# Optimization experiments

Measured on AMD Instinct MI355X. Metric: run time of the kernel, lower is better.

The kernel has to match this reference:

```python
import jax, jax.numpy as jnp
import numpy as np

SR = 24000
N_FFT = 2048
WIN = 960
HOP = 240
NUM_BANDS = 150
HID = 128
OUT = 64
LOG_E_MIN = -18.0  # stands in for trained log_energy_min buffer
LOG_E_MAX = 5.0    # stands in for trained log_energy_max buffer
FREQ_INTERVAL = SR / N_FFT


def _stft_power(x):
    # torchaudio Spectrogram(power=2, center=True, pad_mode=reflect)
    pad = N_FFT // 2
    xp = jnp.pad(x, ((0, 0), (pad, pad)), mode='reflect')
    n = jnp.arange(WIN, dtype=jnp.float32)
    win = 0.5 - 0.5 * jnp.cos(2.0 * jnp.pi * n / WIN)  # periodic hann
    lp = (N_FFT - WIN) // 2
    win = jnp.pad(win, (lp, N_FFT - WIN - lp))  # center-pad window to n_fft
    T = 1 + x.shape[1] // HOP
    idx = (jnp.arange(T) * HOP)[:, None] + jnp.arange(N_FFT)[None, :]  # [T, n_fft]
    frames = xp[:, idx] * win  # [B, T, n_fft]
    F = jnp.fft.rfft(frames, axis=-1)  # [B, T, n_fft//2+1]
    return F.real ** 2 + F.imag ** 2


def _lstm_dir(feat_tbd, w_ih, w_hh, b, reverse):
    # feat_tbd: [T, B, D]; PyTorch gate order i, f, g, o
    xs = jnp.flip(feat_tbd, 0) if reverse else feat_tbd
    pre = jnp.einsum('tbd,gd->tbg', xs, w_ih) + b  # input projection hoisted out of scan

    def step(carry, z_in):
        h, c = carry
        z = z_in + h @ w_hh.T
        i, f, g, o = jnp.split(z, 4, axis=-1)
        c = jax.nn.sigmoid(f) * c + jax.nn.sigmoid(i) * jnp.tanh(g)
        h = jax.nn.sigmoid(o) * jnp.tanh(c)
        return (h, c), h

    B = feat_tbd.shape[1]
    h0 = jnp.zeros((B, HID), feat_tbd.dtype)
    _, hs = jax.lax.scan(step, (h0, h0), pre)
    return jnp.flip(hs, 0) if reverse else hs


def setup_inputs() -> dict:
    key = jax.random.key(0)
    ks = jax.random.split(key, 12)
    B, L, T = 16, 240000, 1001
    x = jax.random.normal(ks[0], (B, L), jnp.float32) * 0.1
    f0_raw = jax.random.uniform(ks[1], (B, T), jnp.float32, 50.0, 400.0)
    voiced = jax.random.uniform(ks[2], (B, T)) > 0.1
    f0 = jnp.where(voiced, f0_raw, 0.0)
    D_in = NUM_BANDS * 2 + 1  # 301
    s = 0.08
    return {
        'x': x,
        'f0': f0,
        'w_ih_f': jax.random.normal(ks[3], (4 * HID, D_in), jnp.float32) * s,
        'w_hh_f': jax.random.normal(ks[4], (4 * HID, HID), jnp.float32) * s,
        'b_f': jax.random.normal(ks[5], (4 * HID,), jnp.float32) * s,
        'w_ih_b': jax.random.normal(ks[6], (4 * HID, D_in), jnp.float32) * s,
        'w_hh_b': jax.random.normal(ks[7], (4 * HID, HID), jnp.float32) * s,
        'b_b': jax.random.normal(ks[8], (4 * HID,), jnp.float32) * s,
        'ln_g': jnp.ones((2 * HID,), jnp.float32),
        'ln_b': jnp.zeros((2 * HID,), jnp.float32),
        'out_w': jax.random.normal(ks[9], (OUT, 2 * HID), jnp.float32) * 0.02,
        'out_b': jnp.zeros((OUT,), jnp.float32),
    }


def reference(x, f0, w_ih_f, w_hh_f, b_f, w_ih_b, w_hh_b, b_b, ln_g, ln_b, out_w, out_b):
    spec = _stft_power(x)                     # [B, T, 1025]
    spec = spec.at[..., -1].set(0.0)          # spec[..., -1] = 0
    Tf = min(spec.shape[1], f0.shape[1])
    spec = spec[:, :Tf]
    f0 = f0[:, :Tf]
    f0_nonzero = jnp.where(f0 > 0, f0, SR / NUM_BANDS * 0.5)
    mult = jnp.arange(1.0, NUM_BANDS + 0.5, 0.5, dtype=jnp.float32)  # [299]
    harms = f0_nonzero[..., None] * mult                              # [B, T, 299]
    harms = jnp.concatenate([harms[..., :1] * 0.5, harms], axis=-1)   # [B, T, 300]
    hidx = jnp.clip(jnp.round(harms / FREQ_INTERVAL).astype(jnp.int32), 0, spec.shape[-1] - 1)
    harms_energy = jnp.take_along_axis(spec, hidx, axis=-1)           # irregular gather
    log_energy = jnp.log(harms_energy + 1e-8)
    feature = (log_energy - LOG_E_MIN) / (LOG_E_MAX - LOG_E_MIN)
    feature = jnp.concatenate([feature, jnp.log(f0_nonzero)[..., None]], axis=-1)  # [B, T, 301]
    ft = feature.transpose(1, 0, 2)  # [T, B, 301]
    hf = _lstm_dir(ft, w_ih_f, w_hh_f, b_f, False)
    hb = _lstm_dir(ft, w_ih_b, w_hh_b, b_b, True)
    h = jnp.concatenate([hf, hb], axis=-1).transpose(1, 0, 2)  # [B, T, 256]
    mu = h.mean(-1, keepdims=True)
    var = h.var(-1, keepdims=True)
    hn = (h - mu) / jnp.sqrt(var + 1e-5) * ln_g + ln_b
    return hn @ out_w.T + out_b  # [B, T, 64]
```

## Files before the change

kernel.cpp:

```cpp
#include <hip/hip_runtime.h>

typedef __bf16 bf16x8 __attribute__((ext_vector_type(8)));
typedef float f32x4 __attribute__((ext_vector_type(4)));
typedef int   i32x4 __attribute__((ext_vector_type(4)));

__device__ __forceinline__ void sync_lds() {
    asm volatile("s_waitcnt lgkmcnt(0)" ::: "memory");
    __builtin_amdgcn_s_barrier();
}

__global__ __launch_bounds__(256) void prep_kernel(
    const float* __restrict__ x, const float* __restrict__ w_ih_f, const float* __restrict__ w_ih_b,
    __bf16* __restrict__ BT, __bf16* __restrict__ A, __bf16* __restrict__ WT)
{
    int blk = blockIdx.x;
    if (blk < 7680) {
        int id = blk * 256 + threadIdx.x;
        int n = id / 960;
        int j = id - n * 960;
        int k = n >> 1;
        int p = (k * (544 + j)) & 2047;
        float pr = (float)p * (1.0f / 2048.0f);
        float v = (n & 1) ? __builtin_amdgcn_sinf(pr) : __builtin_amdgcn_cosf(pr);
        BT[id] = (__bf16)v;
    } else if (blk < 37920) {
        int id = (blk - 7680) * 256 + threadIdx.x;
        int frame = id / 480;
        int jp = (id - frame * 480) * 2;
        float v[2] = {0.f, 0.f};
        if (frame < 16016) {
            int b = frame / 1001;
            int t = frame - b * 1001;
            const float* xb = x + (size_t)b * 240000;
            #pragma unroll
            for (int e = 0; e < 2; ++e) {
                int j = jp + e;
                int s = t * 240 + j - 480;
                if (s < 0) s = -s;
                else if (s >= 240000) s = 479998 - s;
                float win = 0.5f - 0.5f * __builtin_amdgcn_cosf((float)j * (1.0f / 960.0f));
                v[e] = xb[s] * win;
            }
        }
        union { unsigned int u; __bf16 h[2]; } pk;
        pk.h[0] = (__bf16)v[0]; pk.h[1] = (__bf16)v[1];
        *reinterpret_cast<unsigned int*>(&A[(size_t)frame * 960 + jp]) = pk.u;
    } else {
        int id = (blk - 37920) * 256 + threadIdx.x;
        int n = id / 320;
        int k = id - n * 320;
        float v = 0.f;
        if (k < 301) v = (n < 512) ? w_ih_f[n * 301 + k] : w_ih_b[(n - 512) * 301 + k];
        WT[id] = (__bf16)v;
    }
}

__global__ __launch_bounds__(256) void gemm_kernel(
    const __bf16* __restrict__ A, const __bf16* __restrict__ BT,
    int Ka, int kIters, int mode,
    __bf16* __restrict__ Cdft, float* __restrict__ pre,
    const float* __restrict__ b_f, const float* __restrict__ b_b)
{
    __shared__ __bf16 As[128 * 64];
    __shared__ __bf16 Bs[128 * 64];
    const int tid = threadIdx.x;
    const int wave = tid >> 6, lane = tid & 63, l15 = lane & 15, quad = lane >> 4;
    const int bn = blockIdx.x, bm = blockIdx.y;
    const int qm = wave >> 1, qn = wave & 1;
    f32x4 acc[4][4] = {};
    const int rl  = lane >> 3;
    const int gch = (lane & 7) ^ rl;
    const __bf16* Ag = A + (size_t)(bm * 128) * Ka;
    const __bf16* Bg = BT + (size_t)(bn * 128) * Ka;

    for (int kb = 0; kb < kIters; ++kb) {
        int k0 = kb * 64;
        #pragma unroll
        for (int p = 0; p < 4; ++p) {
            int c = wave + p * 4;
            int row = c * 8 + rl;
            __builtin_amdgcn_global_load_lds(
                (const __attribute__((address_space(1))) void*)(Ag + (size_t)row * Ka + k0 + gch * 8),
                (__attribute__((address_space(3))) void*)(As + c * 512), 16, 0, 0);
            __builtin_amdgcn_global_load_lds(
                (const __attribute__((address_space(1))) void*)(Bg + (size_t)row * Ka + k0 + gch * 8),
                (__attribute__((address_space(3))) void*)(Bs + c * 512), 16, 0, 0);
        }
        __syncthreads();
        #pragma unroll
        for (int ks = 0; ks < 2; ++ks) {
            bf16x8 af[4], bfr[4];
            #pragma unroll
            for (int i = 0; i < 4; ++i) {
                int row = qm * 64 + i * 16 + l15;
                int ch = (ks * 4 + quad) ^ (l15 & 7);
                af[i] = *reinterpret_cast<const bf16x8*>(&As[row * 64 + ch * 8]);
            }
            #pragma unroll
            for (int j = 0; j < 4; ++j) {
                int row = qn * 64 + j * 16 + l15;
                int ch = (ks * 4 + quad) ^ (l15 & 7);
                bfr[j] = *reinterpret_cast<const bf16x8*>(&Bs[row * 64 + ch * 8]);
            }
            #pragma unroll
            for (int i = 0; i < 4; ++i)
                #pragma unroll
                for (int j = 0; j < 4; ++j)
                    acc[i][j] = __builtin_amdgcn_mfma_f32_16x16x32_bf16(af[i], bfr[j], acc[i][j], 0, 0, 0);
        }
        __syncthreads();
    }

    if (mode == 0) {
        #pragma unroll
        for (int i = 0; i < 4; ++i)
            #pragma unroll
            for (int j = 0; j < 4; ++j) {
                int n = bn * 128 + qn * 64 + j * 16 + l15;
                #pragma unroll
                for (int r = 0; r < 4; ++r) {
                    int m = bm * 128 + qm * 64 + i * 16 + quad * 4 + r;
                    Cdft[(size_t)m * 2048 + n] = (__bf16)acc[i][j][r];
                }
            }
    } else {
        const float L2E = 1.4426950408889634f;
        for (int i = 0; i < 4; ++i)
            for (int j = 0; j < 4; ++j) {
                int n = bn * 128 + qn * 64 + j * 16 + l15;
                float bias = (n < 512) ? b_f[n] : b_b[n - 512];
                int dirg = n >> 9;
                int ngate = n & 511;
                int g = ngate >> 7;
                int jj = ngate & 127;
                float gam = (g == 2) ? (-2.f * L2E) : (-L2E);
                for (int r = 0; r < 4; ++r) {
                    int m = bm * 128 + qm * 64 + i * 16 + quad * 4 + r;
                    if (m < 16016) {
                        int b = m / 1001;
                        int t = m - b * 1001;
                        size_t off = ((size_t)(t * 2 + dirg) * 16 + b) * 512 + jj * 4 + g;
                        pre[off] = gam * (acc[i][j][r] + bias);
                    }
                }
            }
    }
}

__global__ __launch_bounds__(256) void build_feat(const float* __restrict__ f0,
    const __bf16* __restrict__ Cdft, __bf16* __restrict__ feat)
{
    __shared__ __bf16 row[2048];
    const int frame = blockIdx.x;
    const int tid = threadIdx.x;
    __builtin_amdgcn_global_load_lds(
        (const __attribute__((address_space(1))) void*)(Cdft + (size_t)frame * 2048 + tid * 8),
        (__attribute__((address_space(3))) void*)(row + (tid >> 6) * 512), 16, 0, 0);

    int b = frame / 1001;
    int t = frame - b * 1001;
    float f0v = f0[b * 1001 + t];
    float f0nz = (f0v > 0.f) ? f0v : 80.f;
    __syncthreads();

    const float LN2 = 0.6931471805599453f;
    for (int d = tid; d < 320; d += 256) {
        float val = 0.f;
        if (d < 300) {
            float mult = (d == 0) ? 0.5f : (float)(d + 1) * 0.5f;
            int kidx = (int)rintf(f0nz * mult * (1.0f / 11.71875f));
            kidx = min(max(kidx, 0), 1024);
            float e = 0.f;
            if (kidx < 1024) {
                union { unsigned int u; __bf16 h[2]; } c;
                c.u = *reinterpret_cast<const unsigned int*>(&row[2 * kidx]);
                float c0 = (float)c.h[0], c1 = (float)c.h[1];
                e = c0 * c0 + c1 * c1;
            }
            val = (__builtin_amdgcn_logf(e + 1e-8f) * LN2 + 18.f) * (1.f / 23.f);
        } else if (d == 300) {
            val = __builtin_amdgcn_logf(f0nz) * LN2;
        }
        feat[(size_t)frame * 320 + d] = (__bf16)val;
    }
}

__global__ __launch_bounds__(256) void lstm_kernel(
    const float* __restrict__ w_hh_f, const float* __restrict__ w_hh_b,
    const float* __restrict__ pre, float* __restrict__ h_out)
{
    const int bid = blockIdx.x;
    const int b   = bid & 15;
    const int dir = bid >> 4;
    const float* w_hh = dir ? w_hh_b : w_hh_f;
    const int tid = threadIdx.x;
    const int wave = tid >> 6, lane = tid & 63, l15 = lane & 15, quad = lane >> 4;
    const bool own = ((l15 & 1) == 0);
    const int cellj = wave * 32 + ((l15 >> 1) << 2) + quad;
    const int m0 = (l15 >> 1) & 1, m1 = (l15 >> 2) & 1, m2 = (l15 >> 3) & 1;

    __shared__ __attribute__((aligned(16))) signed char h8[2][128];

    i32x4 afrag[8][2];
    #pragma unroll
    for (int mt = 0; mt < 8; ++mt) {
        int s = wave * 128 + mt * 16 + l15;
        const float* wrow = w_hh + (size_t)((s & 3) * 128 + (s >> 2)) * 128;
        #pragma unroll
        for (int kt = 0; kt < 2; ++kt) {
            i32x4 v;
            #pragma unroll
            for (int d = 0; d < 4; ++d) {
                int pk = 0;
                #pragma unroll
                for (int bi = 0; bi < 4; ++bi) {
                    int k = kt * 64 + quad * 16 + d * 4 + bi;
                    int q = (int)rintf(wrow[k] * 254.f);
                    pk |= (q & 255) << (bi * 8);
                }
                v[d] = pk;
            }
            afrag[mt][kt] = v;
        }
    }

    if (tid < 64) reinterpret_cast<int*>(h8)[tid] = 0;

    const int t0 = dir ? 1000 : 0;
    const ptrdiff_t pre_sstride  = dir ? -16384 : 16384;
    const ptrdiff_t hout_sstride = dir ? -2048  : 2048;
    const float* pre_base = pre + ((size_t)(t0 * 2 + dir) * 16 + b) * 512 + (size_t)cellj * 4;
    float* hout_base = h_out + (((size_t)dir * 1001 + t0) * 16 + b) * 128 + cellj;

    float cstate = 0.f;
    const float L2E = 1.4426950408889634f;
    const float DF = 1.0f / (254.f * 127.f);
    const float CI = -L2E * DF;
    const float CG = -2.f * L2E * DF;

    auto body = [&](int s, f32x4 P) {
        const signed char* hb = h8[s & 1];
        i32x4 b0 = *reinterpret_cast<const i32x4*>(&hb[quad * 16]);
        i32x4 b1 = *reinterpret_cast<const i32x4*>(&hb[64 + quad * 16]);

        i32x4 acc[8] = {};
        #pragma unroll
        for (int mt = 0; mt < 8; ++mt)
            acc[mt] = __builtin_amdgcn_mfma_i32_16x16x64_i8(afrag[mt][0], b0, acc[mt], 0, 0, 0);
        #pragma unroll
        for (int mt = 0; mt < 8; ++mt)
            acc[mt] = __builtin_amdgcn_mfma_i32_16x16x64_i8(afrag[mt][1], b1, acc[mt], 0, 0, 0);

        i32x4 ta = m0 ? acc[1] : acc[0];
        i32x4 tb = m0 ? acc[3] : acc[2];
        i32x4 tc = m0 ? acc[5] : acc[4];
        i32x4 td = m0 ? acc[7] : acc[6];
        i32x4 ua = m1 ? tb : ta;
        i32x4 ub = m1 ? td : tc;
        i32x4 z4 = m2 ? ub : ua;

        float ai = fmaf((float)z4[0], CI, P[0]);
        float af_ = fmaf((float)z4[1], CI, P[1]);
        float ag = fmaf((float)z4[2], CG, P[2]);
        float ao = fmaf((float)z4[3], CI, P[3]);
        float A = __builtin_amdgcn_exp2f(ai);
        float B = __builtin_amdgcn_exp2f(af_);
        float C = __builtin_amdgcn_exp2f(ag);
        float D = __builtin_amdgcn_exp2f(ao);
        float Pp = (1.f + A) * (1.f + C);
        float Q = 1.f + B;
        float cn = (cstate * Pp + (1.f - C) * Q) * __builtin_amdgcn_rcpf(Pp * Q);
        cstate = cn;
        float E = __builtin_amdgcn_exp2f(-2.f * L2E * cn);
        float h = (1.f - E) * __builtin_amdgcn_rcpf((1.f + D) * (1.f + E));

        if (own) {
            h8[(s + 1) & 1][cellj] = (signed char)(int)rintf(h * 127.f);
            hout_base[(ptrdiff_t)s * hout_sstride] = h;
        }
    };

    auto load_pre = [&](int sidx) -> f32x4 {
        return *reinterpret_cast<const f32x4*>(pre_base + (ptrdiff_t)sidx * pre_sstride);
    };

    f32x4 P0 = load_pre(0), P1 = load_pre(1), P2 = load_pre(2), P3 = load_pre(3);
    __syncthreads();

    for (int s = 0; s < 1000; s += 4) {
        body(s, P0);     P0 = load_pre(s + 4); sync_lds();
        body(s + 1, P1); P1 = load_pre(s + 5); sync_lds();
        body(s + 2, P2); P2 = load_pre(s + 6); sync_lds();
        body(s + 3, P3); P3 = load_pre(s + 7); sync_lds();
    }
    body(1000, P0);
}

__global__ __launch_bounds__(256) void out_kernel(
    const float* __restrict__ h_out, const float* __restrict__ ln_g, const float* __restrict__ ln_b,
    const float* __restrict__ out_w, const float* __restrict__ out_b, float* __restrict__ out)
{
    __shared__ __bf16 hn_lds[16 * 264];
    const int tid = threadIdx.x;
    const int wave = tid >> 6, lane = tid & 63, l15 = lane & 15, quad = lane >> 4;

    float lg0 = ln_g[lane],        lb0 = ln_b[lane];
    float lg1 = ln_g[64 + lane],   lb1 = ln_b[64 + lane];
    float lg2 = ln_g[128 + lane],  lb2 = ln_b[128 + lane];
    float lg3 = ln_g[192 + lane],  lb3 = ln_b[192 + lane];

    #pragma unroll
    for (int rr = 0; rr < 4; ++rr) {
        int wrow = wave * 4 + rr;
        int r = blockIdx.x * 16 + wrow;
        int b = r / 1001, t = r - b * 1001;
        size_t basef = ((size_t)t * 16 + b) * 128;
        size_t baseb = ((size_t)(1001 + t) * 16 + b) * 128;
        float h0 = h_out[basef + lane];
        float h1 = h_out[basef + 64 + lane];
        float h2 = h_out[baseb + lane];
        float h3 = h_out[baseb + 64 + lane];
        float s1 = h0 + h1 + h2 + h3;
        float s2 = h0 * h0 + h1 * h1 + h2 * h2 + h3 * h3;
        #pragma unroll
        for (int m = 32; m >= 1; m >>= 1) {
            s1 += __shfl_xor(s1, m, 64);
            s2 += __shfl_xor(s2, m, 64);
        }
        float mu = s1 * (1.f / 256.f);
        float var = s2 * (1.f / 256.f) - mu * mu;
        float rstd = rsqrtf(var + 1e-5f);
        hn_lds[wrow * 264 + lane]       = (__bf16)((h0 - mu) * rstd * lg0 + lb0);
        hn_lds[wrow * 264 + 64 + lane]  = (__bf16)((h1 - mu) * rstd * lg1 + lb1);
        hn_lds[wrow * 264 + 128 + lane] = (__bf16)((h2 - mu) * rstd * lg2 + lb2);
        hn_lds[wrow * 264 + 192 + lane] = (__bf16)((h3 - mu) * rstd * lg3 + lb3);
    }
    __syncthreads();

    const int o = wave * 16 + l15;
    f32x4 accA = {}, accB = {};
    #pragma unroll
    for (int kt = 0; kt < 8; ++kt) {
        bf16x8 a = *reinterpret_cast<const bf16x8*>(&hn_lds[l15 * 264 + kt * 32 + quad * 8]);
        const float* wp = out_w + (size_t)o * 256 + kt * 32 + quad * 8;
        bf16x8 bv;
        #pragma unroll
        for (int e = 0; e < 8; ++e) bv[e] = (__bf16)wp[e];
        if (kt & 1) accB = __builtin_amdgcn_mfma_f32_16x16x32_bf16(a, bv, accB, 0, 0, 0);
        else        accA = __builtin_amdgcn_mfma_f32_16x16x32_bf16(a, bv, accA, 0, 0, 0);
    }
    f32x4 acc = accA + accB;
    float ob = out_b[o];
    #pragma unroll
    for (int rc = 0; rc < 4; ++rc) {
        int r = blockIdx.x * 16 + quad * 4 + rc;
        out[(size_t)r * 64 + o] = acc[rc] + ob;
    }
}

extern "C" void kernel_launch(void* const* d_in, const int* in_sizes, int n_in,
                              void* d_out, int out_size, void* d_ws, size_t ws_size,
                              hipStream_t stream) {
    const float* x      = (const float*)d_in[0];
    const float* f0     = (const float*)d_in[1];
    const float* w_ih_f = (const float*)d_in[2];
    const float* w_hh_f = (const float*)d_in[3];
    const float* b_f    = (const float*)d_in[4];
    const float* w_ih_b = (const float*)d_in[5];
    const float* w_hh_b = (const float*)d_in[6];
    const float* b_b    = (const float*)d_in[7];
    const float* ln_g   = (const float*)d_in[8];
    const float* ln_b   = (const float*)d_in[9];
    const float* out_w  = (const float*)d_in[10];
    const float* out_b  = (const float*)d_in[11];
    float* out = (float*)d_out;

    char* ws = (char*)d_ws;
    size_t off = 0;
    auto alloc = [&](size_t bytes) { size_t o = off; off = (off + bytes + 255) & ~(size_t)255; return o; };
    __bf16* A     = (__bf16*)(ws + alloc((size_t)16128 * 960 * 2));
    __bf16* BT    = (__bf16*)(ws + alloc((size_t)2048 * 960 * 2));
    __bf16* Cdft  = (__bf16*)(ws + alloc((size_t)16128 * 2048 * 2));
    __bf16* feat  = (__bf16*)(ws + alloc((size_t)16128 * 320 * 2));
    __bf16* WT    = (__bf16*)(ws + alloc((size_t)1024 * 320 * 2));
    float*  preA  = (float*)(ws + alloc((size_t)(1001 * 2 + 16) * 16 * 512 * 4));
    float*  pre   = preA + (size_t)8 * 16 * 512;
    float*  h_out = (float*)(ws + alloc((size_t)2 * 1001 * 16 * 128 * 4));
    (void)ws_size; (void)in_sizes; (void)n_in; (void)out_size;

    prep_kernel <<<39200, 256, 0, stream>>>(x, w_ih_f, w_ih_b, BT, A, WT);
    gemm_kernel <<<dim3(16, 126), 256, 0, stream>>>(A, BT, 960, 15, 0, Cdft, nullptr, nullptr, nullptr);
    build_feat  <<<16016, 256, 0, stream>>>(f0, Cdft, feat);
    gemm_kernel <<<dim3(8, 126), 256, 0, stream>>>(feat, WT, 320, 5, 1, nullptr, pre, b_f, b_b);
    lstm_kernel <<<32, 256, 0, stream>>>(w_hh_f, w_hh_b, pre, h_out);
    out_kernel  <<<1001, 256, 0, stream>>>(h_out, ln_g, ln_b, out_w, out_b, out);
}
```

Baseline: 618.3 us.

## Replace MFMA int8 recurrent matvec with per-lane sdot4 dot products

The LSTM recurrent h·W_hh product moves off the int8 MFMA instructions and onto scalar-vector sdot4 dot products. Each lane pair owns one cell and holds that cell's 4 gate rows for half of K, and the two halves are combined with a ds_swizzle. This removes the MFMA latency chain and the select tree used to extract each cell's gate values on every serial timestep. The cost is 64 sdot4 instructions per lane per step and 64 packed weight registers per lane.

```diff
diff --git a/kernel.cpp b/kernel.cpp
--- a/kernel.cpp
+++ b/kernel.cpp
@@ -194,33 +194,27 @@
     const int dir = bid >> 4;
     const float* w_hh = dir ? w_hh_b : w_hh_f;
     const int tid = threadIdx.x;
-    const int wave = tid >> 6, lane = tid & 63, l15 = lane & 15, quad = lane >> 4;
-    const bool own = ((l15 & 1) == 0);
-    const int cellj = wave * 32 + ((l15 >> 1) << 2) + quad;
-    const int m0 = (l15 >> 1) & 1, m1 = (l15 >> 2) & 1, m2 = (l15 >> 3) & 1;
+    const int wave = tid >> 6, lane = tid & 63;
+    const int cell = wave * 32 + (lane >> 1);
+    const int kh   = lane & 1;
+    const int base_k = kh * 64;
+    const bool own = (kh == 0);
 
     __shared__ __attribute__((aligned(16))) signed char h8[2][128];
 
-    i32x4 afrag[8][2];
+    int wpk[4][16];
     #pragma unroll
-    for (int mt = 0; mt < 8; ++mt) {
-        int s = wave * 128 + mt * 16 + l15;
-        const float* wrow = w_hh + (size_t)((s & 3) * 128 + (s >> 2)) * 128;
-        #pragma unroll
-        for (int kt = 0; kt < 2; ++kt) {
-            i32x4 v;
-            #pragma unroll
-            for (int d = 0; d < 4; ++d) {
-                int pk = 0;
-                #pragma unroll
-                for (int bi = 0; bi < 4; ++bi) {
-                    int k = kt * 64 + quad * 16 + d * 4 + bi;
-                    int q = (int)rintf(wrow[k] * 254.f);
-                    pk |= (q & 255) << (bi * 8);
-                }
-                v[d] = pk;
-            }
-            afrag[mt][kt] = v;
+    for (int g = 0; g < 4; ++g) {
+        const float* wrow = w_hh + (size_t)(g * 128 + cell) * 128 + base_k;
+        #pragma unroll
+        for (int d = 0; d < 16; ++d) {
+            int pk = 0;
+            #pragma unroll
+            for (int bi = 0; bi < 4; ++bi) {
+                int q = (int)rintf(wrow[d * 4 + bi] * 254.f);
+                pk |= (q & 255) << (bi * 8);
+            }
+            wpk[g][d] = pk;
         }
     }
 
@@ -229,8 +223,8 @@
     const int t0 = dir ? 1000 : 0;
     const ptrdiff_t pre_sstride  = dir ? -16384 : 16384;
     const ptrdiff_t hout_sstride = dir ? -2048  : 2048;
-    const float* pre_base = pre + ((size_t)(t0 * 2 + dir) * 16 + b) * 512 + (size_t)cellj * 4;
-    float* hout_base = h_out + (((size_t)dir * 1001 + t0) * 16 + b) * 128 + cellj;
+    const float* pre_base = pre + ((size_t)(t0 * 2 + dir) * 16 + b) * 512 + (size_t)cell * 4;
+    float* hout_base = h_out + (((size_t)dir * 1001 + t0) * 16 + b) * 128 + cell;
 
     float cstate = 0.f;
     const float L2E = 1.4426950408889634f;
@@ -240,29 +234,31 @@
 
     auto body = [&](int s, f32x4 P) {
         const signed char* hb = h8[s & 1];
-        i32x4 b0 = *reinterpret_cast<const i32x4*>(&hb[quad * 16]);
-        i32x4 b1 = *reinterpret_cast<const i32x4*>(&hb[64 + quad * 16]);
-
-        i32x4 acc[8] = {};
-        #pragma unroll
-        for (int mt = 0; mt < 8; ++mt)
-            acc[mt] = __builtin_amdgcn_mfma_i32_16x16x64_i8(afrag[mt][0], b0, acc[mt], 0, 0, 0);
-        #pragma unroll
-        for (int mt = 0; mt < 8; ++mt)
-            acc[mt] = __builtin_amdgcn_mfma_i32_16x16x64_i8(afrag[mt][1], b1, acc[mt], 0, 0, 0);
-
-        i32x4 ta = m0 ? acc[1] : acc[0];
-        i32x4 tb = m0 ? acc[3] : acc[2];
-        i32x4 tc = m0 ? acc[5] : acc[4];
-        i32x4 td = m0 ? acc[7] : acc[6];
-        i32x4 ua = m1 ? tb : ta;
-        i32x4 ub = m1 ? td : tc;
-        i32x4 z4 = m2 ? ub : ua;
-
-        float ai = fmaf((float)z4[0], CI, P[0]);
-        float af_ = fmaf((float)z4[1], CI, P[1]);
-        float ag = fmaf((float)z4[2], CG, P[2]);
-        float ao = fmaf((float)z4[3], CI, P[3]);
+        i32x4 hv[4];
+        #pragma unroll
+        for (int q = 0; q < 4; ++q)
+            hv[q] = *reinterpret_cast<const i32x4*>(hb + base_k + q * 16);
+
+        int z0 = 0, z1 = 0, z2 = 0, z3 = 0;
+        #pragma unroll
+        for (int q = 0; q < 4; ++q)
+            #pragma unroll
+            for (int d = 0; d < 4; ++d) {
+                int hvd = hv[q][d];
+                z0 = __builtin_amdgcn_sdot4(wpk[0][q * 4 + d], hvd, z0, false);
+                z1 = __builtin_amdgcn_sdot4(wpk[1][q * 4 + d], hvd, z1, false);
+                z2 = __builtin_amdgcn_sdot4(wpk[2][q * 4 + d], hvd, z2, false);
+                z3 = __builtin_amdgcn_sdot4(wpk[3][q * 4 + d], hvd, z3, false);
+            }
+        z0 += __builtin_amdgcn_ds_swizzle(z0, 0x041F);
+        z1 += __builtin_amdgcn_ds_swizzle(z1, 0x041F);
+        z2 += __builtin_amdgcn_ds_swizzle(z2, 0x041F);
+        z3 += __builtin_amdgcn_ds_swizzle(z3, 0x041F);
+
+        float ai  = fmaf((float)z0, CI, P[0]);
+        float af_ = fmaf((float)z1, CI, P[1]);
+        float ag  = fmaf((float)z2, CG, P[2]);
+        float ao  = fmaf((float)z3, CI, P[3]);
         float A = __builtin_amdgcn_exp2f(ai);
         float B = __builtin_amdgcn_exp2f(af_);
         float C = __builtin_amdgcn_exp2f(ag);
@@ -275,7 +271,7 @@
         float h = (1.f - E) * __builtin_amdgcn_rcpf((1.f + D) * (1.f + E));
 
         if (own) {
-            h8[(s + 1) & 1][cellj] = (signed char)(int)rintf(h * 127.f);
+            h8[(s + 1) & 1][cell] = (signed char)(int)rintf(h * 127.f);
             hout_base[(ptrdiff_t)s * hout_sstride] = h;
         }
     };
```

New measurement: 636.9 us. +3.0%, slower.
